# Kernel optimization log

Hardware: AMD Instinct MI355X
Metric: run time of the kernel (lower is better)

Reference implementation:

```python
import jax, jax.numpy as jnp
import numpy as np

B, H, W = 16, 16, 16
L = 32          # in_capsules
O = 32          # out_capsules
P = 16          # p_size
PD = 4          # p_dim = sqrt(p_size)
ETA = 1.0


def setup_inputs() -> dict:
    key = jax.random.key(0)
    k1, k2, k3 = jax.random.split(key, 3)
    # [B, H, W, L*(P+1)]: first L*P channels are poses, last L are activations in [0,1]
    input_tensor = jax.random.uniform(k1, (B, H, W, L * (P + 1)), dtype=jnp.float32)
    # transform weights: [L, O, 4, 4] (kernel_size=1, shared over spatial positions)
    weights = jax.random.normal(k2, (L, O, PD, PD), dtype=jnp.float32) / np.sqrt(PD)
    activation_bias = jax.random.uniform(k3, (O,), dtype=jnp.float32)
    return {"input_tensor": input_tensor, "weights": weights,
            "activation_bias": activation_bias}


def reference(input_tensor, weights, activation_bias):
    Bs, Hh, Ww, _ = input_tensor.shape
    M = Hh * Ww
    # split poses / activations
    poses = input_tensor[..., : L * P].reshape(Bs, M, L, PD, PD)   # [B, M, L, 4, 4]
    acts = input_tensor[..., L * P:].reshape(Bs, M * L)            # [B, N]
    # votes[b, (m,l), o] = pose[b,m,l] @ W[l,o]  (shared transform, repeated over M)
    votes = jnp.einsum('bmlij,lojk->bmloik', poses, weights)
    votes = votes.reshape(Bs, M * L, O, P)                         # [B, N, O, 16]
    # weight votes by input activations and group per output capsule
    Y = (acts[:, :, None, None] * votes).transpose(0, 2, 1, 3)     # [B, O, N, 16]
    # top-1 right singular vector via gram matrix eigendecomposition (detached)
    gram = jnp.einsum('bonp,bonq->bopq', Y, Y)                     # [B, O, 16, 16]
    _, V = jnp.linalg.eigh(jax.lax.stop_gradient(gram))            # ascending eigvals
    pose_out = V[..., -1]                                          # [B, O, 16]
    # agreement: ||Y u||^2 / ||Y||_F^2
    yu = jnp.einsum('bonp,bop->bon', Y, pose_out)                  # [B, O, N]
    ratio = (yu ** 2).sum(-1) / (Y ** 2).sum((-1, -2))             # [B, O]
    act_out = jax.nn.sigmoid(ETA * (ratio - activation_bias))      # [B, O]
    return act_out, pose_out
```

## Files before the change

kernel.cpp:

```cpp
#include <hip/hip_runtime.h>

#define B_ 16
#define L_ 32
#define O_ 32
#define M_ 256
#define CH_ 544


__device__ __forceinline__ float rl(float v, int lane) {
  return __int_as_float(__builtin_amdgcn_readlane(__float_as_int(v), lane));
}

__device__ __forceinline__ float sum16_rl(float v) {
  float s = rl(v, 0);
#pragma unroll
  for (int j = 1; j < 16; j++) s += rl(v, j);
  return s;
}

__device__ __forceinline__ float frcp(float x) { return __builtin_amdgcn_rcpf(x); }
__device__ __forceinline__ float frsq(float x) { return __builtin_amdgcn_rsqf(x); }


__device__ __forceinline__ float slapy2f(float x, float y) {
  float xa = fabsf(x), ya = fabsf(y);
  float w = fmaxf(xa, ya), z = fminf(xa, ya);
  float q = z * frcp(w);
  float res = w * sqrtf(1.f + q * q);
  return (z == 0.f) ? w : res;
}

__device__ __forceinline__ void slartgf(float f, float g, float* c, float* s, float* r) {
  float t = f * f + g * g;
  float inv = frsq(t);
  float d = t * inv;
  float cg = fabsf(f) * inv;
  float rg = copysignf(d, f);
  float sg = g * copysignf(inv, f);
  bool g0 = (g == 0.f), f0 = (f == 0.f);
  *c = g0 ? 1.f : (f0 ? 0.f : cg);
  *s = g0 ? 0.f : (f0 ? copysignf(1.f, g) : sg);
  *r = g0 ? f : (f0 ? fabsf(g) : rg);
}

__device__ __forceinline__ void slaev2f(float a, float b, float c,
                                        float* rt1, float* rt2, float* cs1, float* sn1) {
  float sm = a + c, df = a - c;
  float adf = fabsf(df);
  float tb = b + b;
  float ab = fabsf(tb);
  float acmx, acmn;
  if (fabsf(a) > fabsf(c)) { acmx = a; acmn = c; } else { acmx = c; acmn = a; }
  float rt;
  if (adf > ab) { float q = ab / adf; rt = adf * sqrtf(1.f + q * q); }
  else if (adf < ab) { float q = adf / ab; rt = ab * sqrtf(1.f + q * q); }
  else rt = ab * sqrtf(2.f);
  int sgn1;
  if (sm < 0.f) { *rt1 = 0.5f * (sm - rt); sgn1 = -1; *rt2 = (acmx / *rt1) * acmn - (b / *rt1) * b; }
  else if (sm > 0.f) { *rt1 = 0.5f * (sm + rt); sgn1 = 1; *rt2 = (acmx / *rt1) * acmn - (b / *rt1) * b; }
  else { *rt1 = 0.5f * rt; *rt2 = -0.5f * rt; sgn1 = 1; }
  float cs; int sgn2;
  if (df >= 0.f) { cs = df + rt; sgn2 = 1; } else { cs = df - rt; sgn2 = -1; }
  float acs = fabsf(cs), c1, s1;
  if (acs > ab) { float ct = -tb / cs; s1 = 1.f / sqrtf(1.f + ct * ct); c1 = ct * s1; }
  else if (ab == 0.f) { c1 = 1.f; s1 = 0.f; }
  else { float tn = -cs / tb; c1 = 1.f / sqrtf(1.f + tn * tn); s1 = tn * c1; }
  if (sgn1 == sgn2) { float tn = c1; c1 = -s1; s1 = tn; }
  *cs1 = c1; *sn1 = s1;
}

__global__ __launch_bounds__(256) void moments_kernel(const float* __restrict__ in,
                                                      float* __restrict__ Tmom) {
  int bl = blockIdx.x;
  int b = bl >> 5, l = bl & 31;
  int t = threadIdx.x;
  int w = t >> 6, lane = t & 63;
  __shared__ __align__(16) float ut[4][16][68];
  __shared__ float red[4][16][16];
  const float* base = in + (size_t)b * (M_ * CH_);
  const float* row = base + (size_t)(w * 64 + lane) * CH_ + l * 16;
  float4 p0 = *(const float4*)(row + 0);
  float4 p1 = *(const float4*)(row + 4);
  float4 p2 = *(const float4*)(row + 8);
  float4 p3 = *(const float4*)(row + 12);
  float a = row[512 - l * 16 + l];
  float (*u)[68] = ut[w];
  u[0][lane] = a * p0.x;  u[1][lane] = a * p0.y;  u[2][lane] = a * p0.z;  u[3][lane] = a * p0.w;
  u[4][lane] = a * p1.x;  u[5][lane] = a * p1.y;  u[6][lane] = a * p1.z;  u[7][lane] = a * p1.w;
  u[8][lane] = a * p2.x;  u[9][lane] = a * p2.y;  u[10][lane] = a * p2.z; u[11][lane] = a * p2.w;
  u[12][lane] = a * p3.x; u[13][lane] = a * p3.y; u[14][lane] = a * p3.z; u[15][lane] = a * p3.w;
  asm volatile("" ::: "memory");
  int c = lane & 15, r0 = lane >> 4;
  float acc0 = 0.f, acc1 = 0.f, acc2 = 0.f, acc3 = 0.f;
#pragma unroll
  for (int m4 = 0; m4 < 64; m4 += 4) {
    float4 cv = *(const float4*)&u[c][m4];
    float4 a0 = *(const float4*)&u[r0][m4];
    float4 a1 = *(const float4*)&u[r0 + 4][m4];
    float4 a2 = *(const float4*)&u[r0 + 8][m4];
    float4 a3 = *(const float4*)&u[r0 + 12][m4];
    acc0 += a0.x * cv.x + a0.y * cv.y + a0.z * cv.z + a0.w * cv.w;
    acc1 += a1.x * cv.x + a1.y * cv.y + a1.z * cv.z + a1.w * cv.w;
    acc2 += a2.x * cv.x + a2.y * cv.y + a2.z * cv.z + a2.w * cv.w;
    acc3 += a3.x * cv.x + a3.y * cv.y + a3.z * cv.z + a3.w * cv.w;
  }
  red[w][r0][c] = acc0;
  red[w][r0 + 4][c] = acc1;
  red[w][r0 + 8][c] = acc2;
  red[w][r0 + 12][c] = acc3;
  __syncthreads();
  int rr_ = t >> 4, cc_ = t & 15;
  float s = (red[0][rr_][cc_] + red[1][rr_][cc_]) + (red[2][rr_][cc_] + red[3][rr_][cc_]);
  Tmom[bl * 256 + t] = s;
}

__global__ __launch_bounds__(64) void gram_eig_kernel(const float* __restrict__ Tmom,
                                                      const float* __restrict__ Wt,
                                                      const float* __restrict__ bias,
                                                      float* __restrict__ out) {
  int bo = blockIdx.x;
  int b = bo >> 5, o = bo & 31;
  int lane = threadIdx.x;

  __shared__ __align__(16) float4 Wall4[128];
  __shared__ __align__(16) float4 Tsh4[4 * 18];
  __shared__ float A[16][17];
  __shared__ __align__(16) float Zt[16][16];

  float biasv = bias[o];

  const float4* Wt4 = (const float4*)Wt;
#pragma unroll
  for (int k = 0; k < 2; k++) {
    int idx = lane + 64 * k;
    int l = idx >> 2, part = idx & 3;
    Wall4[idx] = Wt4[(l * 32 + o) * 4 + part];
  }
  asm volatile("" ::: "memory");

  int p = lane >> 2;
  int i_ = p >> 2, k_ = p & 3;
  int i2 = lane & 3;
  float gx = 0.f, gy = 0.f, gz = 0.f, gw = 0.f;
  const float4* T4 = (const float4*)(Tmom + (size_t)(b * 32) * 256);
  const float* WallF = (const float*)Wall4;
  float4 t0 = T4[0 * 64 + lane], t1 = T4[1 * 64 + lane];
  float4 t2 = T4[2 * 64 + lane], t3 = T4[3 * 64 + lane];
  for (int l = 0; l < 32; l++) {
    Tsh4[(lane >> 4) * 18 + (lane & 15)] = t0;
    asm volatile("" ::: "memory");
    t0 = t1; t1 = t2; t2 = t3;
    if (l + 4 < 32) t3 = T4[(l + 4) * 64 + lane];
    float4 wq0 = Wall4[l * 4 + 0], wq1 = Wall4[l * 4 + 1];
    float4 wq2 = Wall4[l * 4 + 2], wq3 = Wall4[l * 4 + 3];
#pragma unroll
    for (int jj = 0; jj < 4; jj++) {
      float4 trow = Tsh4[i_ * 18 + jj * 4 + i2];
      float ux = trow.x * wq0.x + trow.y * wq1.x + trow.z * wq2.x + trow.w * wq3.x;
      float uy = trow.x * wq0.y + trow.y * wq1.y + trow.z * wq2.y + trow.w * wq3.y;
      float uz = trow.x * wq0.z + trow.y * wq1.z + trow.z * wq2.z + trow.w * wq3.z;
      float uw = trow.x * wq0.w + trow.y * wq1.w + trow.z * wq2.w + trow.w * wq3.w;
      float wk = WallF[l * 16 + jj * 4 + k_];
      gx += wk * ux; gy += wk * uy; gz += wk * uz; gw += wk * uw;
    }
    asm volatile("" ::: "memory");
  }
  {
    int q0 = i2 * 4;
    A[p][q0 + 0] = gx; A[p][q0 + 1] = gy; A[p][q0 + 2] = gz; A[p][q0 + 3] = gw;
  }
  asm volatile("" ::: "memory");

  int c16 = lane & 15;
  float a[16];
#pragma unroll
  for (int r = 0; r < 16; r++) a[r] = A[r][c16];

  float trace;
  {
    float diag = 0.f;
#pragma unroll
    for (int r = 0; r < 16; r++) if (c16 == r) diag = a[r];
    trace = sum16_rl((lane < 16) ? diag : 0.f);
  }

  float dreg = 0.f, ereg = 0.f, taureg = 0.f;
  float hv[14];
#pragma unroll
  for (int i = 0; i < 15; i++) {
    float cn = 0.f;
#pragma unroll
    for (int r = i + 2; r < 16; r++) cn += a[r] * a[r];
    float xn2 = rl(cn, i);
    float alpha = rl(a[i + 1], i);
    float taui = 0.f;
    float vc = 0.f;
    if (xn2 == 0.f) {
      if (lane == i) ereg = alpha;
    } else {
      float xnorm = sqrtf(xn2);
      float beta = -copysignf(slapy2f(alpha, xnorm), alpha);
      taui = (beta - alpha) / beta;
      float rs = 1.f / (alpha - beta);
      if (lane == i) ereg = beta;
      vc = (lane == i + 1) ? 1.f : ((lane >= i + 2 && lane < 16) ? a[i] * rs : 0.f);
      float vb[16];
#pragma unroll
      for (int r = i + 1; r < 16; r++) vb[r] = rl(vc, r);
      float acc = 0.f;
#pragma unroll
      for (int r = i + 1; r < 16; r++) acc += a[r] * vb[r];
      float wc = (lane >= i + 1 && lane < 16) ? taui * acc : 0.f;
      float wb[16];
#pragma unroll
      for (int r = i + 1; r < 16; r++) wb[r] = rl(wc, r);
      float dot = 0.f;
#pragma unroll
      for (int r = i + 1; r < 16; r++) dot += vb[r] * wb[r];
      float alph2 = -0.5f * taui * dot;
      wc += alph2 * vc;
#pragma unroll
      for (int r = i + 1; r < 16; r++) wb[r] += alph2 * vb[r];
#pragma unroll
      for (int r = i + 1; r < 16; r++) a[r] -= vb[r] * wc + wb[r] * vc;
    }
    if (i < 14) hv[i] = vc;
    if (lane == i) taureg = taui;
  }
#pragma unroll
  for (int r = 0; r < 16; r++) if (c16 == r) dreg = a[r];
  if (lane >= 16) dreg = 0.f;

  float z[16];
#pragma unroll
  for (int r = 0; r < 16; r++) z[r] = (lane == r) ? 1.f : 0.f;
#pragma unroll
  for (int i = 13; i >= 0; i--) {
    float taui = rl(taureg, i);
    if (taui != 0.f) {
      float vbq[16];
      float s = 0.f;
#pragma unroll
      for (int r = i + 1; r < 16; r++) { vbq[r] = rl(hv[i], r); s += vbq[r] * z[r]; }
      s *= taui;
#pragma unroll
      for (int r = i + 1; r < 16; r++) z[r] -= vbq[r] * s;
    }
  }
  if (lane < 16) {
    float4* zt4 = (float4*)&Zt[lane][0];
    zt4[0] = make_float4(z[0], z[1], z[2], z[3]);
    zt4[1] = make_float4(z[4], z[5], z[6], z[7]);
    zt4[2] = make_float4(z[8], z[9], z[10], z[11]);
    zt4[3] = make_float4(z[12], z[13], z[14], z[15]);
  }
  asm volatile("" ::: "memory");

  float zz[16];
#pragma unroll
  for (int k2 = 0; k2 < 16; k2++) zz[k2] = Zt[k2][c16];

  const float eps = 5.9604645e-08f;
  const float eps2 = eps * eps;
  const float safmin = 1.17549435e-38f;
  int l1 = 0, jtot = 0;
  const int nmaxit = 480;
  float dsh = __shfl(dreg, (lane + 1) & 63, 64);

  while (l1 < 16) {
    if (l1 > 0) { if (lane == l1 - 1) ereg = 0.f; }
    bool co = (lane < 15) &&
              ((ereg == 0.f) ||
               (fabsf(ereg) <= __builtin_amdgcn_sqrtf(fabsf(dreg)) *
                                   __builtin_amdgcn_sqrtf(fabsf(dsh)) * eps));
    unsigned long long bm = __ballot(co) & ~((1ull << l1) - 1ull);
    int m = bm ? (__ffsll(bm) - 1) : 15;
    if (m < 15) { if (lane == m) ereg = 0.f; }
    int l = l1, lend = m;
    l1 = m + 1;
    if (lend == l) continue;
    {
      float dl = rl(dreg, l), dle = rl(dreg, lend);
      if (fabsf(dle) < fabsf(dl)) { int tq = l; l = lend; lend = tq; }
    }

    if (lend > l) {
      for (;;) {
        bool cj = (lane < 15) && ((ereg * ereg) <= eps2 * fabsf(dreg) * fabsf(dsh) + safmin);
        int mq;
        if (l != lend) {
          unsigned long long bb2 = __ballot(cj) & ((1ull << lend) - 1ull) & ~((1ull << l) - 1ull);
          mq = bb2 ? (__ffsll(bb2) - 1) : lend;
        } else mq = lend;
        if (mq < lend) { if (lane == mq) ereg = 0.f; }
        if (mq == l) { l++; if (l <= lend) continue; break; }
        if (mq == l + 1) {
          float d_l = rl(dreg, l), e_l = rl(ereg, l), d_l1 = rl(dreg, l + 1);
          float rt1, rt2, cc, ss;
          slaev2f(d_l, e_l, d_l1, &rt1, &rt2, &cc, &ss);
#pragma unroll
          for (int k = 0; k < 15; k++) if (k == l) {
            float z1 = zz[k + 1], z0v = zz[k];
            zz[k + 1] = cc * z1 - ss * z0v;
            zz[k] = ss * z1 + cc * z0v;
          }
          if (lane == l) { dreg = rt1; ereg = 0.f; dsh = rt2; }
          if (lane == l + 1) dreg = rt2;
          if (lane == l - 1) dsh = rt1;
          l += 2; if (l <= lend) continue; break;
        }
        if (jtot == nmaxit) break;
        jtot++;
        float d0 = dreg, e0 = ereg;
        float pp = rl(d0, l);
        float e_lv = rl(e0, l);
        float gg = (rl(d0, l + 1) - pp) * 0.5f * frcp(e_lv);
        float rr = slapy2f(gg, 1.f);
        gg = rl(d0, mq) - pp + e_lv * frcp(gg + copysignf(rr, gg));
        float ss_ = 1.f, cc_ = 1.f;
        pp = 0.f;
#pragma unroll
        for (int i = 14; i >= 0; i--) {
          if (i <= mq - 1 && i >= l) {
            float e_i = rl(e0, i), d_i = rl(d0, i), d_i1 = rl(d0, i + 1);
            float ff = ss_ * e_i, bb = cc_ * e_i;
            slartgf(gg, ff, &cc_, &ss_, &rr);
            if (i != mq - 1) { if (lane == i + 1) ereg = rr; }
            gg = d_i1 - pp;
            rr = (d_i - gg) * ss_ + 2.f * cc_ * bb;
            pp = ss_ * rr;
            float dnew = gg + pp;
            if (lane == i + 1) dreg = dnew;
            if (lane == i) dsh = dnew;
            gg = cc_ * rr - bb;
            float z1 = zz[i + 1], z0v = zz[i];
            zz[i + 1] = cc_ * z1 + ss_ * z0v;
            zz[i] = -ss_ * z1 + cc_ * z0v;
          }
        }
        float dlv = rl(d0, l) - pp;
        if (lane == l) { dreg = dlv; ereg = gg; }
        if (lane == l - 1) dsh = dlv;
      }
    } else {
      for (;;) {
        bool cj = (lane < 15) && ((ereg * ereg) <= eps2 * fabsf(dreg) * fabsf(dsh) + safmin);
        int mq;
        if (l != lend) {
          unsigned long long bb2 = __ballot(cj) & ((1ull << l) - 1ull) & ~((1ull << lend) - 1ull);
          mq = bb2 ? (63 - __clzll(bb2) + 1) : lend;
        } else mq = lend;
        if (mq > lend) { if (lane == mq - 1) ereg = 0.f; }
        if (mq == l) { l--; if (l >= lend) continue; break; }
        if (mq == l - 1) {
          float d_lm1 = rl(dreg, l - 1), e_lm1 = rl(ereg, l - 1), d_l = rl(dreg, l);
          float rt1, rt2, cc, ss;
          slaev2f(d_lm1, e_lm1, d_l, &rt1, &rt2, &cc, &ss);
#pragma unroll
          for (int k = 0; k < 15; k++) if (k == l - 1) {
            float z1 = zz[k + 1], z0v = zz[k];
            zz[k + 1] = cc * z1 - ss * z0v;
            zz[k] = ss * z1 + cc * z0v;
          }
          if (lane == l - 1) { dreg = rt1; ereg = 0.f; dsh = rt2; }
          if (lane == l) dreg = rt2;
          if (lane == l - 2) dsh = rt1;
          l -= 2; if (l >= lend) continue; break;
        }
        if (jtot == nmaxit) break;
        jtot++;
        float d0 = dreg, e0 = ereg;
        float pp = rl(d0, l);
        float e_lm1 = rl(e0, l - 1);
        float gg = (rl(d0, l - 1) - pp) * 0.5f * frcp(e_lm1);
        float rr = slapy2f(gg, 1.f);
        gg = rl(d0, mq) - pp + e_lm1 * frcp(gg + copysignf(rr, gg));
        float ss_ = 1.f, cc_ = 1.f;
        pp = 0.f;
#pragma unroll
        for (int i = 0; i <= 14; i++) {
          if (i >= mq && i <= l - 1) {
            float e_i = rl(e0, i), d_i = rl(d0, i), d_i1 = rl(d0, i + 1);
            float ff = ss_ * e_i, bb = cc_ * e_i;
            slartgf(gg, ff, &cc_, &ss_, &rr);
            if (i != mq) { if (lane == i - 1) ereg = rr; }
            gg = d_i - pp;
            rr = (d_i1 - gg) * ss_ + 2.f * cc_ * bb;
            pp = ss_ * rr;
            float dnew = gg + pp;
            if (lane == i) dreg = dnew;
            if (lane == i - 1) dsh = dnew;
            gg = cc_ * rr - bb;
            float z1 = zz[i + 1], z0v = zz[i];
            zz[i + 1] = cc_ * z1 - ss_ * z0v;
            zz[i] = ss_ * z1 + cc_ * z0v;
          }
        }
        float dlv = rl(d0, l) - pp;
        if (lane == l) dreg = dlv;
        if (lane == l - 1) { ereg = gg; dsh = dlv; }
      }
    }
  }

  float mx = rl(dreg, 0);
  int k = 0;
#pragma unroll
  for (int j = 1; j < 16; j++) {
    float dj = rl(dreg, j);
    if (dj > mx) { mx = dj; k = j; }
  }
  float ratio = mx / trace;
  float act = 1.f / (1.f + expf(-(ratio - biasv)));
  float zk = zz[0];
#pragma unroll
  for (int j = 1; j < 16; j++) zk = (k == j) ? zz[j] : zk;
  if (lane < 16) out[512 + bo * 16 + lane] = zk;
  if (lane == 0) out[bo] = act;
}

extern "C" void kernel_launch(void* const* d_in, const int* in_sizes, int n_in,
                              void* d_out, int out_size, void* d_ws, size_t ws_size,
                              hipStream_t stream) {
  const float* in = (const float*)d_in[0];
  const float* w = (const float*)d_in[1];
  const float* bias = (const float*)d_in[2];
  float* out = (float*)d_out;
  float* Tmom = (float*)d_ws;

  moments_kernel<<<B_ * L_, 256, 0, stream>>>(in, Tmom);
  gram_eig_kernel<<<B_ * O_, 64, 0, stream>>>(Tmom, w, bias, out);
}
```

Before: 131.1 us.

## Preload all moments into LDS and force wave-uniform branches in eigen solver

Stages all 32 moment tiles into shared memory up front instead of a rolling four-deep register prefetch, which removes per-iteration LDS store/barrier pairs from the gram accumulation loop. Wraps branch conditions in the tridiagonalization and QL/QR iteration with readfirstlane so the compiler emits scalar branches instead of divergent exec-mask code. Makes slaev2f noinline and returns a float4 to cut code size and register pressure. The larger LDS footprint (about 37KB) and the function-call overhead are the trade-offs.

```diff
diff --git a/kernel.cpp b/kernel.cpp
--- a/kernel.cpp
+++ b/kernel.cpp
@@ -17,6 +17,8 @@
   for (int j = 1; j < 16; j++) s += rl(v, j);
   return s;
 }
+
+__device__ __forceinline__ int uni(int c) { return __builtin_amdgcn_readfirstlane(c); }
 
 __device__ __forceinline__ float frcp(float x) { return __builtin_amdgcn_rcpf(x); }
 __device__ __forceinline__ float frsq(float x) { return __builtin_amdgcn_rsqf(x); }
@@ -34,17 +36,16 @@
   float t = f * f + g * g;
   float inv = frsq(t);
   float d = t * inv;
-  float cg = fabsf(f) * inv;
+  float cg_ = fabsf(f) * inv;
   float rg = copysignf(d, f);
   float sg = g * copysignf(inv, f);
   bool g0 = (g == 0.f), f0 = (f == 0.f);
-  *c = g0 ? 1.f : (f0 ? 0.f : cg);
+  *c = g0 ? 1.f : (f0 ? 0.f : cg_);
   *s = g0 ? 0.f : (f0 ? copysignf(1.f, g) : sg);
   *r = g0 ? f : (f0 ? fabsf(g) : rg);
 }
 
-__device__ __forceinline__ void slaev2f(float a, float b, float c,
-                                        float* rt1, float* rt2, float* cs1, float* sn1) {
+__device__ __noinline__ float4 slaev2f(float a, float b, float c) {
   float sm = a + c, df = a - c;
   float adf = fabsf(df);
   float tb = b + b;
@@ -55,10 +56,11 @@
   if (adf > ab) { float q = ab / adf; rt = adf * sqrtf(1.f + q * q); }
   else if (adf < ab) { float q = adf / ab; rt = ab * sqrtf(1.f + q * q); }
   else rt = ab * sqrtf(2.f);
+  float rt1, rt2;
   int sgn1;
-  if (sm < 0.f) { *rt1 = 0.5f * (sm - rt); sgn1 = -1; *rt2 = (acmx / *rt1) * acmn - (b / *rt1) * b; }
-  else if (sm > 0.f) { *rt1 = 0.5f * (sm + rt); sgn1 = 1; *rt2 = (acmx / *rt1) * acmn - (b / *rt1) * b; }
-  else { *rt1 = 0.5f * rt; *rt2 = -0.5f * rt; sgn1 = 1; }
+  if (sm < 0.f) { rt1 = 0.5f * (sm - rt); sgn1 = -1; rt2 = (acmx / rt1) * acmn - (b / rt1) * b; }
+  else if (sm > 0.f) { rt1 = 0.5f * (sm + rt); sgn1 = 1; rt2 = (acmx / rt1) * acmn - (b / rt1) * b; }
+  else { rt1 = 0.5f * rt; rt2 = -0.5f * rt; sgn1 = 1; }
   float cs; int sgn2;
   if (df >= 0.f) { cs = df + rt; sgn2 = 1; } else { cs = df - rt; sgn2 = -1; }
   float acs = fabsf(cs), c1, s1;
@@ -66,7 +68,7 @@
   else if (ab == 0.f) { c1 = 1.f; s1 = 0.f; }
   else { float tn = -cs / tb; c1 = 1.f / sqrtf(1.f + tn * tn); s1 = tn * c1; }
   if (sgn1 == sgn2) { float tn = c1; c1 = -s1; s1 = tn; }
-  *cs1 = c1; *sn1 = s1;
+  return make_float4(rt1, rt2, c1, s1);
 }
 
 __global__ __launch_bounds__(256) void moments_kernel(const float* __restrict__ in,
@@ -123,7 +125,7 @@
   int lane = threadIdx.x;
 
   __shared__ __align__(16) float4 Wall4[128];
-  __shared__ __align__(16) float4 Tsh4[4 * 18];
+  __shared__ __align__(16) float4 Tall4[32 * 72];
   __shared__ float A[16][17];
   __shared__ __align__(16) float Zt[16][16];
 
@@ -136,26 +138,25 @@
     int l = idx >> 2, part = idx & 3;
     Wall4[idx] = Wt4[(l * 32 + o) * 4 + part];
   }
+  const float4* T4 = (const float4*)(Tmom + (size_t)(b * 32) * 256);
+  int soff = (lane >> 4) * 18 + (lane & 15);
+#pragma unroll
+  for (int l = 0; l < 32; l++) {
+    Tall4[l * 72 + soff] = T4[l * 64 + lane];
+  }
   asm volatile("" ::: "memory");
 
   int p = lane >> 2;
   int i_ = p >> 2, k_ = p & 3;
   int i2 = lane & 3;
   float gx = 0.f, gy = 0.f, gz = 0.f, gw = 0.f;
-  const float4* T4 = (const float4*)(Tmom + (size_t)(b * 32) * 256);
   const float* WallF = (const float*)Wall4;
-  float4 t0 = T4[0 * 64 + lane], t1 = T4[1 * 64 + lane];
-  float4 t2 = T4[2 * 64 + lane], t3 = T4[3 * 64 + lane];
   for (int l = 0; l < 32; l++) {
-    Tsh4[(lane >> 4) * 18 + (lane & 15)] = t0;
-    asm volatile("" ::: "memory");
-    t0 = t1; t1 = t2; t2 = t3;
-    if (l + 4 < 32) t3 = T4[(l + 4) * 64 + lane];
     float4 wq0 = Wall4[l * 4 + 0], wq1 = Wall4[l * 4 + 1];
     float4 wq2 = Wall4[l * 4 + 2], wq3 = Wall4[l * 4 + 3];
 #pragma unroll
     for (int jj = 0; jj < 4; jj++) {
-      float4 trow = Tsh4[i_ * 18 + jj * 4 + i2];
+      float4 trow = Tall4[l * 72 + i_ * 18 + jj * 4 + i2];
       float ux = trow.x * wq0.x + trow.y * wq1.x + trow.z * wq2.x + trow.w * wq3.x;
       float uy = trow.x * wq0.y + trow.y * wq1.y + trow.z * wq2.y + trow.w * wq3.y;
       float uz = trow.x * wq0.z + trow.y * wq1.z + trow.z * wq2.z + trow.w * wq3.z;
@@ -163,7 +164,6 @@
       float wk = WallF[l * 16 + jj * 4 + k_];
       gx += wk * ux; gy += wk * uy; gz += wk * uz; gw += wk * uw;
     }
-    asm volatile("" ::: "memory");
   }
   {
     int q0 = i2 * 4;
@@ -195,7 +195,7 @@
     float alpha = rl(a[i + 1], i);
     float taui = 0.f;
     float vc = 0.f;
-    if (xn2 == 0.f) {
+    if (uni(xn2 == 0.f ? 1 : 0)) {
       if (lane == i) ereg = alpha;
     } else {
       float xnorm = sqrtf(xn2);
@@ -237,7 +237,7 @@
 #pragma unroll
   for (int i = 13; i >= 0; i--) {
     float taui = rl(taureg, i);
-    if (taui != 0.f) {
+    if (uni(taui != 0.f ? 1 : 0)) {
       float vbq[16];
       float s = 0.f;
 #pragma unroll
@@ -267,7 +267,7 @@
   const int nmaxit = 480;
   float dsh = __shfl(dreg, (lane + 1) & 63, 64);
 
-  while (l1 < 16) {
+  while (uni(l1 < 16 ? 1 : 0)) {
     if (l1 > 0) { if (lane == l1 - 1) ereg = 0.f; }
     bool co = (lane < 15) &&
               ((ereg == 0.f) ||
@@ -278,13 +278,13 @@
     if (m < 15) { if (lane == m) ereg = 0.f; }
     int l = l1, lend = m;
     l1 = m + 1;
-    if (lend == l) continue;
+    if (uni(lend == l ? 1 : 0)) continue;
     {
       float dl = rl(dreg, l), dle = rl(dreg, lend);
       if (fabsf(dle) < fabsf(dl)) { int tq = l; l = lend; lend = tq; }
     }
 
-    if (lend > l) {
+    if (uni(lend > l ? 1 : 0)) {
       for (;;) {
         bool cj = (lane < 15) && ((ereg * ereg) <= eps2 * fabsf(dreg) * fabsf(dsh) + safmin);
         int mq;
@@ -293,13 +293,12 @@
           mq = bb2 ? (__ffsll(bb2) - 1) : lend;
         } else mq = lend;
         if (mq < lend) { if (lane == mq) ereg = 0.f; }
-        if (mq == l) { l++; if (l <= lend) continue; break; }
-        if (mq == l + 1) {
-          float d_l = rl(dreg, l), e_l = rl(ereg, l), d_l1 = rl(dreg, l + 1);
-          float rt1, rt2, cc, ss;
-          slaev2f(d_l, e_l, d_l1, &rt1, &rt2, &cc, &ss);
-#pragma unroll
-          for (int k = 0; k < 15; k++) if (k == l) {
+        if (uni(mq == l ? 1 : 0)) { l++; if (uni(l <= lend ? 1 : 0)) continue; break; }
+        if (uni(mq == l + 1 ? 1 : 0)) {
+          float4 ev = slaev2f(rl(dreg, l), rl(ereg, l), rl(dreg, l + 1));
+          float rt1 = ev.x, rt2 = ev.y, cc = ev.z, ss = ev.w;
+#pragma unroll
+          for (int k = 0; k < 15; k++) if (uni(k == l ? 1 : 0)) {
             float z1 = zz[k + 1], z0v = zz[k];
             zz[k + 1] = cc * z1 - ss * z0v;
             zz[k] = ss * z1 + cc * z0v;
@@ -307,9 +306,9 @@
           if (lane == l) { dreg = rt1; ereg = 0.f; dsh = rt2; }
           if (lane == l + 1) dreg = rt2;
           if (lane == l - 1) dsh = rt1;
-          l += 2; if (l <= lend) continue; break;
+          l += 2; if (uni(l <= lend ? 1 : 0)) continue; break;
         }
-        if (jtot == nmaxit) break;
+        if (uni(jtot == nmaxit ? 1 : 0)) break;
         jtot++;
         float d0 = dreg, e0 = ereg;
         float pp = rl(d0, l);
@@ -321,7 +320,7 @@
         pp = 0.f;
 #pragma unroll
         for (int i = 14; i >= 0; i--) {
-          if (i <= mq - 1 && i >= l) {
+          if (uni((i <= mq - 1 && i >= l) ? 1 : 0)) {
             float e_i = rl(e0, i), d_i = rl(d0, i), d_i1 = rl(d0, i + 1);
             float ff = ss_ * e_i, bb = cc_ * e_i;
             slartgf(gg, ff, &cc_, &ss_, &rr);
@@ -351,13 +350,12 @@
           mq = bb2 ? (63 - __clzll(bb2) + 1) : lend;
         } else mq = lend;
         if (mq > lend) { if (lane == mq - 1) ereg = 0.f; }
-        if (mq == l) { l--; if (l >= lend) continue; break; }
-        if (mq == l - 1) {
-          float d_lm1 = rl(dreg, l - 1), e_lm1 = rl(ereg, l - 1), d_l = rl(dreg, l);
-          float rt1, rt2, cc, ss;
-          slaev2f(d_lm1, e_lm1, d_l, &rt1, &rt2, &cc, &ss);
-#pragma unroll
-          for (int k = 0; k < 15; k++) if (k == l - 1) {
+        if (uni(mq == l ? 1 : 0)) { l--; if (uni(l >= lend ? 1 : 0)) continue; break; }
+        if (uni(mq == l - 1 ? 1 : 0)) {
+          float4 ev = slaev2f(rl(dreg, l - 1), rl(ereg, l - 1), rl(dreg, l));
+          float rt1 = ev.x, rt2 = ev.y, cc = ev.z, ss = ev.w;
+#pragma unroll
+          for (int k = 0; k < 15; k++) if (uni(k == l - 1 ? 1 : 0)) {
             float z1 = zz[k + 1], z0v = zz[k];
             zz[k + 1] = cc * z1 - ss * z0v;
             zz[k] = ss * z1 + cc * z0v;
@@ -365,9 +363,9 @@
           if (lane == l - 1) { dreg = rt1; ereg = 0.f; dsh = rt2; }
           if (lane == l) dreg = rt2;
           if (lane == l - 2) dsh = rt1;
-          l -= 2; if (l >= lend) continue; break;
+          l -= 2; if (uni(l >= lend ? 1 : 0)) continue; break;
         }
-        if (jtot == nmaxit) break;
+        if (uni(jtot == nmaxit ? 1 : 0)) break;
         jtot++;
         float d0 = dreg, e0 = ereg;
         float pp = rl(d0, l);
@@ -379,7 +377,7 @@
         pp = 0.f;
 #pragma unroll
         for (int i = 0; i <= 14; i++) {
-          if (i >= mq && i <= l - 1) {
+          if (uni((i >= mq && i <= l - 1) ? 1 : 0)) {
             float e_i = rl(e0, i), d_i = rl(d0, i), d_i1 = rl(d0, i + 1);
             float ff = ss_ * e_i, bb = cc_ * e_i;
             slartgf(gg, ff, &cc_, &ss_, &rr);
```

Result: slower. 136.1 us (+3.8%).

## Split gram/tridiagonalization and QL eigen-iteration into separate kernels

Applied to the files above, without the earlier changes.

Splits the fused gram+eigensolver kernel into two launches: one builds the gram matrix, tridiagonalizes it and writes Z, d, e and the trace to a workspace. A second kernel runs the implicit QL/QR iteration and writes the outputs. It also makes slaev2f noinline returning a float4, and hoists the readlane broadcasts of d and e into per-sweep arrays. The aim is to lower register pressure in each kernel and cut repeated readlanes in the Givens sweep, at the cost of an extra launch and a global-memory round trip.

```diff
diff --git a/kernel.cpp b/kernel.cpp
--- a/kernel.cpp
+++ b/kernel.cpp
@@ -5,6 +5,7 @@
 #define O_ 32
 #define M_ 256
 #define CH_ 544
+#define WS2_STRIDE 320
 
 
 __device__ __forceinline__ float rl(float v, int lane) {
@@ -34,17 +35,16 @@
   float t = f * f + g * g;
   float inv = frsq(t);
   float d = t * inv;
-  float cg = fabsf(f) * inv;
+  float cg_ = fabsf(f) * inv;
   float rg = copysignf(d, f);
   float sg = g * copysignf(inv, f);
   bool g0 = (g == 0.f), f0 = (f == 0.f);
-  *c = g0 ? 1.f : (f0 ? 0.f : cg);
+  *c = g0 ? 1.f : (f0 ? 0.f : cg_);
   *s = g0 ? 0.f : (f0 ? copysignf(1.f, g) : sg);
   *r = g0 ? f : (f0 ? fabsf(g) : rg);
 }
 
-__device__ __forceinline__ void slaev2f(float a, float b, float c,
-                                        float* rt1, float* rt2, float* cs1, float* sn1) {
+__device__ __noinline__ float4 slaev2f(float a, float b, float c) {
   float sm = a + c, df = a - c;
   float adf = fabsf(df);
   float tb = b + b;
@@ -55,10 +55,11 @@
   if (adf > ab) { float q = ab / adf; rt = adf * sqrtf(1.f + q * q); }
   else if (adf < ab) { float q = adf / ab; rt = ab * sqrtf(1.f + q * q); }
   else rt = ab * sqrtf(2.f);
+  float rt1, rt2;
   int sgn1;
-  if (sm < 0.f) { *rt1 = 0.5f * (sm - rt); sgn1 = -1; *rt2 = (acmx / *rt1) * acmn - (b / *rt1) * b; }
-  else if (sm > 0.f) { *rt1 = 0.5f * (sm + rt); sgn1 = 1; *rt2 = (acmx / *rt1) * acmn - (b / *rt1) * b; }
-  else { *rt1 = 0.5f * rt; *rt2 = -0.5f * rt; sgn1 = 1; }
+  if (sm < 0.f) { rt1 = 0.5f * (sm - rt); sgn1 = -1; rt2 = (acmx / rt1) * acmn - (b / rt1) * b; }
+  else if (sm > 0.f) { rt1 = 0.5f * (sm + rt); sgn1 = 1; rt2 = (acmx / rt1) * acmn - (b / rt1) * b; }
+  else { rt1 = 0.5f * rt; rt2 = -0.5f * rt; sgn1 = 1; }
   float cs; int sgn2;
   if (df >= 0.f) { cs = df + rt; sgn2 = 1; } else { cs = df - rt; sgn2 = -1; }
   float acs = fabsf(cs), c1, s1;
@@ -66,7 +67,7 @@
   else if (ab == 0.f) { c1 = 1.f; s1 = 0.f; }
   else { float tn = -cs / tb; c1 = 1.f / sqrtf(1.f + tn * tn); s1 = tn * c1; }
   if (sgn1 == sgn2) { float tn = c1; c1 = -s1; s1 = tn; }
-  *cs1 = c1; *sn1 = s1;
+  return make_float4(rt1, rt2, c1, s1);
 }
 
 __global__ __launch_bounds__(256) void moments_kernel(const float* __restrict__ in,
@@ -114,10 +115,9 @@
   Tmom[bl * 256 + t] = s;
 }
 
-__global__ __launch_bounds__(64) void gram_eig_kernel(const float* __restrict__ Tmom,
-                                                      const float* __restrict__ Wt,
-                                                      const float* __restrict__ bias,
-                                                      float* __restrict__ out) {
+__global__ __launch_bounds__(64) void gram_sytd2_kernel(const float* __restrict__ Tmom,
+                                                        const float* __restrict__ Wt,
+                                                        float* __restrict__ ws2) {
   int bo = blockIdx.x;
   int b = bo >> 5, o = bo & 31;
   int lane = threadIdx.x;
@@ -125,9 +125,6 @@
   __shared__ __align__(16) float4 Wall4[128];
   __shared__ __align__(16) float4 Tsh4[4 * 18];
   __shared__ float A[16][17];
-  __shared__ __align__(16) float Zt[16][16];
-
-  float biasv = bias[o];
 
   const float4* Wt4 = (const float4*)Wt;
 #pragma unroll
@@ -247,25 +244,43 @@
       for (int r = i + 1; r < 16; r++) z[r] -= vbq[r] * s;
     }
   }
+
+  float* basep = ws2 + (size_t)bo * WS2_STRIDE;
   if (lane < 16) {
-    float4* zt4 = (float4*)&Zt[lane][0];
-    zt4[0] = make_float4(z[0], z[1], z[2], z[3]);
-    zt4[1] = make_float4(z[4], z[5], z[6], z[7]);
-    zt4[2] = make_float4(z[8], z[9], z[10], z[11]);
-    zt4[3] = make_float4(z[12], z[13], z[14], z[15]);
-  }
-  asm volatile("" ::: "memory");
-
+    float4* dst = (float4*)(basep + lane * 16);
+    dst[0] = make_float4(z[0], z[1], z[2], z[3]);
+    dst[1] = make_float4(z[4], z[5], z[6], z[7]);
+    dst[2] = make_float4(z[8], z[9], z[10], z[11]);
+    dst[3] = make_float4(z[12], z[13], z[14], z[15]);
+    basep[256 + lane] = dreg;
+  }
+  if (lane < 15) basep[272 + lane] = ereg;
+  if (lane == 0) basep[288] = trace;
+}
+
+__global__ __launch_bounds__(64) void steqr_kernel(const float* __restrict__ ws2,
+                                                   const float* __restrict__ bias,
+                                                   float* __restrict__ out) {
+  int bo = blockIdx.x;
+  int o = bo & 31;
+  int lane = threadIdx.x;
+  int c16 = lane & 15;
+  const float* basep = ws2 + (size_t)bo * WS2_STRIDE;
+
+  float biasv = bias[o];
+  float trace = basep[288];
   float zz[16];
 #pragma unroll
-  for (int k2 = 0; k2 < 16; k2++) zz[k2] = Zt[k2][c16];
+  for (int k = 0; k < 16; k++) zz[k] = (lane < 16) ? basep[k * 16 + c16] : 0.f;
+  float dreg = (lane < 16) ? basep[256 + lane] : 0.f;
+  float ereg = (lane < 15) ? basep[272 + lane] : 0.f;
+  float dsh = (lane < 15) ? basep[256 + lane + 1] : 0.f;
 
   const float eps = 5.9604645e-08f;
   const float eps2 = eps * eps;
   const float safmin = 1.17549435e-38f;
   int l1 = 0, jtot = 0;
   const int nmaxit = 480;
-  float dsh = __shfl(dreg, (lane + 1) & 63, 64);
 
   while (l1 < 16) {
     if (l1 > 0) { if (lane == l1 - 1) ereg = 0.f; }
@@ -295,9 +310,8 @@
         if (mq < lend) { if (lane == mq) ereg = 0.f; }
         if (mq == l) { l++; if (l <= lend) continue; break; }
         if (mq == l + 1) {
-          float d_l = rl(dreg, l), e_l = rl(ereg, l), d_l1 = rl(dreg, l + 1);
-          float rt1, rt2, cc, ss;
-          slaev2f(d_l, e_l, d_l1, &rt1, &rt2, &cc, &ss);
+          float4 ev = slaev2f(rl(dreg, l), rl(ereg, l), rl(dreg, l + 1));
+          float rt1 = ev.x, rt2 = ev.y, cc = ev.z, ss = ev.w;
 #pragma unroll
           for (int k = 0; k < 15; k++) if (k == l) {
             float z1 = zz[k + 1], z0v = zz[k];
@@ -312,6 +326,11 @@
         if (jtot == nmaxit) break;
         jtot++;
         float d0 = dreg, e0 = ereg;
+        float dArr[16], eArr[15];
+#pragma unroll
+        for (int r = 0; r < 16; r++) dArr[r] = rl(d0, r);
+#pragma unroll
+        for (int r = 0; r < 15; r++) eArr[r] = rl(e0, r);
         float pp = rl(d0, l);
         float e_lv = rl(e0, l);
         float gg = (rl(d0, l + 1) - pp) * 0.5f * frcp(e_lv);
@@ -322,7 +341,7 @@
 #pragma unroll
         for (int i = 14; i >= 0; i--) {
           if (i <= mq - 1 && i >= l) {
-            float e_i = rl(e0, i), d_i = rl(d0, i), d_i1 = rl(d0, i + 1);
+            float e_i = eArr[i], d_i = dArr[i], d_i1 = dArr[i + 1];
             float ff = ss_ * e_i, bb = cc_ * e_i;
             slartgf(gg, ff, &cc_, &ss_, &rr);
             if (i != mq - 1) { if (lane == i + 1) ereg = rr; }
@@ -353,9 +372,8 @@
         if (mq > lend) { if (lane == mq - 1) ereg = 0.f; }
         if (mq == l) { l--; if (l >= lend) continue; break; }
         if (mq == l - 1) {
-          float d_lm1 = rl(dreg, l - 1), e_lm1 = rl(ereg, l - 1), d_l = rl(dreg, l);
-          float rt1, rt2, cc, ss;
-          slaev2f(d_lm1, e_lm1, d_l, &rt1, &rt2, &cc, &ss);
+          float4 ev = slaev2f(rl(dreg, l - 1), rl(ereg, l - 1), rl(dreg, l));
+          float rt1 = ev.x, rt2 = ev.y, cc = ev.z, ss = ev.w;
 #pragma unroll
           for (int k = 0; k < 15; k++) if (k == l - 1) {
             float z1 = zz[k + 1], z0v = zz[k];
@@ -370,6 +388,11 @@
         if (jtot == nmaxit) break;
         jtot++;
         float d0 = dreg, e0 = ereg;
+        float dArr[16], eArr[15];
+#pragma unroll
+        for (int r = 0; r < 16; r++) dArr[r] = rl(d0, r);
+#pragma unroll
+        for (int r = 0; r < 15; r++) eArr[r] = rl(e0, r);
         float pp = rl(d0, l);
         float e_lm1 = rl(e0, l - 1);
         float gg = (rl(d0, l - 1) - pp) * 0.5f * frcp(e_lm1);
@@ -380,7 +403,7 @@
 #pragma unroll
         for (int i = 0; i <= 14; i++) {
           if (i >= mq && i <= l - 1) {
-            float e_i = rl(e0, i), d_i = rl(d0, i), d_i1 = rl(d0, i + 1);
+            float e_i = eArr[i], d_i = dArr[i], d_i1 = dArr[i + 1];
             float ff = ss_ * e_i, bb = cc_ * e_i;
             slartgf(gg, ff, &cc_, &ss_, &rr);
             if (i != mq) { if (lane == i - 1) ereg = rr; }
@@ -427,7 +450,9 @@
   const float* bias = (const float*)d_in[2];
   float* out = (float*)d_out;
   float* Tmom = (float*)d_ws;
+  float* ws2 = (float*)d_ws + 512 * 256;
 
   moments_kernel<<<B_ * L_, 256, 0, stream>>>(in, Tmom);
-  gram_eig_kernel<<<B_ * O_, 64, 0, stream>>>(Tmom, w, bias, out);
-}
+  gram_sytd2_kernel<<<B_ * O_, 64, 0, stream>>>(Tmom, w, ws2);
+  steqr_kernel<<<B_ * O_, 64, 0, stream>>>(ws2, bias, out);
+}
```

Result: slower. 135.0 us (+3.0%).
